# Optimization experiments

Measured on AMD Instinct MI355X. Metric: run time of the kernel, lower is better.

The kernel has to match this reference:

```python
import jax, jax.numpy as jnp
import numpy as np

N = 50000
E = 800000
F = 128
HID = 128
C = 40
GAMMA = 0.1
EPS = 0.1


def gcn(x, theta, src, dst, n):
    # GCNConv (bias=False) with added self-loops and symmetric normalization.
    xw = x @ theta  # [N, d]
    ones = jnp.ones(src.shape[0], dtype=x.dtype)
    deg = jax.ops.segment_sum(ones, dst, num_segments=n) + 1.0  # in-degree incl. self loop
    dinv = jax.lax.rsqrt(deg)
    norm = dinv[src] * dinv[dst]            # [E]
    msg = xw[src] * norm[:, None]           # [E, d]  (dominant memory traffic)
    agg = jax.ops.segment_sum(msg, dst, num_segments=n)
    return agg + xw * (dinv * dinv)[:, None]  # self-loop contribution


def antisym_conv(x, W, bias, theta, src, dst, n):
    # PyG AntiSymmetricConv, num_iters=1, act=tanh, eps=0.1, gamma=0.1
    M = W - W.T - GAMMA * jnp.eye(W.shape[0], dtype=x.dtype)
    h = gcn(x, theta, src, dst, n)
    h = x @ M.T + h + bias
    return x + EPS * jnp.tanh(h)


def setup_inputs() -> dict:
    key = jax.random.key(0)
    ks = jax.random.split(key, 12)
    s = 0.05
    return {
        "x": jax.random.normal(ks[0], (N, F), dtype=jnp.float32),
        "edge_index": jax.random.randint(ks[1], (2, E), 0, N, dtype=jnp.int64)
        if jax.config.jax_enable_x64 else jax.random.randint(ks[1], (2, E), 0, N, dtype=jnp.int32),
        # AntiSymmetricConv 1 (num_features channels)
        "W1": jax.random.normal(ks[2], (F, F), dtype=jnp.float32) * s,
        "b1": jnp.zeros((F,), dtype=jnp.float32),
        "T1": jax.random.normal(ks[3], (F, F), dtype=jnp.float32) * s,
        # AntiSymmetricConv 2 (nhid channels)
        "W2": jax.random.normal(ks[4], (HID, HID), dtype=jnp.float32) * s,
        "b2": jnp.zeros((HID,), dtype=jnp.float32),
        "T2": jax.random.normal(ks[5], (HID, HID), dtype=jnp.float32) * s,
        # Linear layers (torch convention: weight [out, in])
        "lw1": jax.random.normal(ks[6], (HID, F), dtype=jnp.float32) * s,
        "lb1": jnp.zeros((HID,), dtype=jnp.float32),
        "lw2": jax.random.normal(ks[7], (C, HID), dtype=jnp.float32) * s,
        "lb2": jnp.zeros((C,), dtype=jnp.float32),
    }


def reference(x, edge_index, W1, b1, T1, W2, b2, T2, lw1, lb1, lw2, lb2):
    src, dst = edge_index[0], edge_index[1]
    n = x.shape[0]
    # eval mode: dropout is identity
    h = antisym_conv(x, W1, b1, T1, src, dst, n)
    h = jax.nn.relu(h)
    h = h @ lw1.T + lb1
    h = jax.nn.relu(h)
    h = antisym_conv(h, W2, b2, T2, src, dst, n)
    h = jax.nn.relu(h)
    x1 = h
    logits = h @ lw2.T + lb2
    result = jax.nn.log_softmax(logits, axis=-1)
    return (result, x1)
```

## Files before the change

### kernel.cpp

```cpp
#include <hip/hip_runtime.h>
#include <hip/hip_bf16.h>
#include <math.h>

#define GAMMA_ 0.1f
#define EPS_ 0.1f
constexpr int BLK = 256;

typedef __attribute__((ext_vector_type(8))) short short8;
typedef __attribute__((ext_vector_type(4))) float f32x4;
typedef __attribute__((ext_vector_type(2))) float f32x2v;
typedef unsigned char u8;

__device__ inline float bflo(uint u) { union { uint i; float f; } v; v.i = u << 16; return v.f; }
__device__ inline float bfhi(uint u) { union { uint i; float f; } v; v.i = u & 0xffff0000u; return v.f; }
__device__ inline ushort f2bf(float f) {
  union { float f; uint i; } v; v.f = f;
  uint i = v.i;
  return (ushort)((i + 0x7fffu + ((i >> 16) & 1u)) >> 16);
}

#if __has_builtin(__builtin_amdgcn_cvt_pk_f32_fp8) && __has_builtin(__builtin_amdgcn_cvt_pk_fp8_f32)
#define HW_FP8 1
#endif

__device__ inline f32x2v fp8x2_dec_sw(uint raw) {
  f32x2v r;
#pragma unroll
  for (int i = 0; i < 2; ++i) {
    uint b = (raw >> (8 * i)) & 0xffu;
    uint em = b & 0x7fu;
    union { uint u; float f; } o;
    o.u = ((b & 0x80u) << 24) | (0x3C000000u + (em << 20));
    r[i] = (em >= 8u) ? o.f : 0.f;
  }
  return r;
}

__device__ inline f32x2v fp8x2_dec(uint raw) {
#ifdef HW_FP8
  return __builtin_amdgcn_cvt_pk_f32_fp8(raw, false);
#else
  return fp8x2_dec_sw(raw);
#endif
}

__device__ inline uint fp8enc1(float x) {
  union { float f; uint u; } v; v.f = x;
  uint s = (v.u >> 24) & 0x80u;
  uint a = v.u & 0x7fffffffu;
  if (a >= 0x43E00000u) return s | 0x7Eu;
  uint r = a + 0x7FFFFu + ((a >> 20) & 1u);
  if (r < 0x3D800000u) return s;
  return s | (((r - 0x3C000000u) >> 20) & 0x7fu);
}

template<bool HI>
__device__ inline uint fp8x2_enc(float f0, float f1, uint old) {
#ifdef HW_FP8
  return __builtin_amdgcn_cvt_pk_fp8_f32(f0, f1, old, HI);
#else
  uint p = fp8enc1(f0) | (fp8enc1(f1) << 8);
  return HI ? ((old & 0x0000ffffu) | (p << 16)) : ((old & 0xffff0000u) | p);
#endif
}

__global__ void k_count(const int* __restrict__ dst, int* cnt,
                        int* __restrict__ rank, int e) {
  int i = blockIdx.x * BLK + threadIdx.x;
  if (i < e) rank[i] = atomicAdd(&cnt[dst[i]], 1);
}

__global__ void k_scan1(const int* __restrict__ cnt, int* __restrict__ rowp,
                        int* __restrict__ bsum, int n) {
  __shared__ int s[BLK];
  int t = threadIdx.x;
  int i = blockIdx.x * BLK + t;
  int v = (i < n) ? cnt[i] : 0;
  s[t] = v; __syncthreads();
  for (int off = 1; off < BLK; off <<= 1) {
    int u = (t >= off) ? s[t - off] : 0;
    __syncthreads();
    s[t] += u;
    __syncthreads();
  }
  if (i < n) rowp[i] = s[t] - v;
  if (t == BLK - 1) bsum[blockIdx.x] = s[t];
}

__global__ void k_scan2(const int* __restrict__ bsum, int* __restrict__ boff, int nb) {
  __shared__ int s[BLK];
  int t = threadIdx.x;
  int v = (t < nb) ? bsum[t] : 0;
  s[t] = v; __syncthreads();
  for (int off = 1; off < BLK; off <<= 1) {
    int u = (t >= off) ? s[t - off] : 0;
    __syncthreads();
    s[t] += u;
    __syncthreads();
  }
  if (t < nb) boff[t] = s[t] - v;
}

__global__ void k_scan3(const int* __restrict__ boff, int* __restrict__ rowp,
                        const int* __restrict__ cnt, float* __restrict__ dinv,
                        int n, int e) {
  int i = blockIdx.x * BLK + threadIdx.x;
  if (i < n) {
    rowp[i] += boff[blockIdx.x];
    dinv[i] = rsqrtf((float)cnt[i] + 1.0f);
    if (i == 0) rowp[n] = e;
  }
}

__global__ void k_fill(const int* __restrict__ src, const int* __restrict__ dst,
                       const int* __restrict__ rowp, const int* __restrict__ rank,
                       int* __restrict__ csrc, int e) {
  int i = blockIdx.x * BLK + threadIdx.x;
  if (i < e) {
    int d = dst[i];
    csrc[rowp[d] + rank[i]] = src[i];
  }
}

__global__ void k_pack(const float* __restrict__ W1, const float* __restrict__ T1,
                       const float* __restrict__ W2, const float* __restrict__ T2,
                       const float* __restrict__ lw1, const float* __restrict__ lw2,
                       ushort* __restrict__ Bpk1, ushort* __restrict__ Bpk2,
                       ushort* __restrict__ Bpkl, ushort* __restrict__ Bpk2l) {
  int idx = blockIdx.x * BLK + threadIdx.x;
  if (idx < 65536) {
    int which = idx >> 15;
    int e = idx & 32767;
    int k = e >> 8, c = e & 255;
    const float* W = which ? W2 : W1;
    const float* T = which ? T2 : T1;
    float v;
    if (c < 128) {
      v = T[k * 128 + c];
    } else {
      int cc = c - 128;
      v = W[cc * 128 + k] - W[k * 128 + cc] - ((cc == k) ? GAMMA_ : 0.f);
    }
    int kt = k >> 5, q = (k >> 3) & 3, j = k & 7;
    ushort* B = which ? Bpk2 : Bpk1;
    B[(((kt * 4 + q) * 256 + c) << 3) + j] = f2bf(v);
  } else if (idx < 81920) {
    int e = idx - 65536;
    int k = e >> 7, c = e & 127;
    float v = lw1[c * 128 + k];
    int kt = k >> 5, q = (k >> 3) & 3, j = k & 7;
    Bpkl[(((kt * 4 + q) * 128 + c) << 3) + j] = f2bf(v);
  } else {
    int e = idx - 81920;
    if (e < 6144) {
      int k = e / 48, c = e - k * 48;
      float v = (c < 40) ? lw2[c * 128 + k] : 0.f;
      int kt = k >> 5, q = (k >> 3) & 3, j = k & 7;
      Bpk2l[(((kt * 4 + q) * 48 + c) << 3) + j] = f2bf(v);
    }
  }
}

__global__ __launch_bounds__(256) void k_mgemm(
    const float* __restrict__ Av, int nrows,
    const ushort* __restrict__ Bpk, const float* __restrict__ dinv,
    ushort* __restrict__ O1, u8* __restrict__ Oq) {
  __shared__ ushort S[64 * 256];
  const int t = threadIdx.x;
  const int w = t >> 6, l = t & 63;
  const int lr = l & 15, lq = l >> 4;
  const int r0 = blockIdx.x * 64;
#pragma unroll
  for (int it = 0; it < 4; ++it) {
    int chunk = it * 256 + t;
    int row = chunk >> 4, c16 = chunk & 15;
    int gr = min(r0 + row, nrows - 1);
    ushort* p = S + row * 128 + (c16 ^ (row & 7)) * 8;
    const float* A = Av + (size_t)gr * 128 + c16 * 8;
    float4 v0 = *(const float4*)(A);
    float4 v1 = *(const float4*)(A + 4);
    ushort4 o0 = {f2bf(v0.x), f2bf(v0.y), f2bf(v0.z), f2bf(v0.w)};
    ushort4 o1 = {f2bf(v1.x), f2bf(v1.y), f2bf(v1.z), f2bf(v1.w)};
    *(ushort4*)(p) = o0;
    *(ushort4*)(p + 4) = o1;
  }
  __syncthreads();
  f32x4 acc[4][4];
#pragma unroll
  for (int rt = 0; rt < 4; ++rt)
#pragma unroll
    for (int n = 0; n < 4; ++n) acc[rt][n] = f32x4{0.f, 0.f, 0.f, 0.f};
#pragma unroll
  for (int kt = 0; kt < 4; ++kt) {
    short8 af[4];
#pragma unroll
    for (int rt = 0; rt < 4; ++rt) {
      int row = rt * 16 + lr;
      af[rt] = *(const short8*)(S + row * 128 + ((kt * 4 + lq) ^ (row & 7)) * 8);
    }
    const ushort* bbase = Bpk + ((size_t)((kt * 4 + lq) * 256) + w * 64 + lr) * 8;
#pragma unroll
    for (int n = 0; n < 4; ++n) {
      short8 bf = *(const short8*)(bbase + n * 16 * 8);
#pragma unroll
      for (int rt = 0; rt < 4; ++rt)
        acc[rt][n] = __builtin_amdgcn_mfma_f32_16x16x32_bf16(af[rt], bf, acc[rt][n], 0, 0, 0);
    }
  }
  __syncthreads();
#pragma unroll
  for (int rt = 0; rt < 4; ++rt)
#pragma unroll
    for (int n = 0; n < 4; ++n)
#pragma unroll
      for (int r = 0; r < 4; ++r) {
        int row = rt * 16 + lq * 4 + r;
        int col = w * 64 + n * 16 + lr;
        int pcol = col ^ (((row >> 2) & 3) << 3);
        S[row * 256 + pcol] = f2bf(acc[rt][n][r]);
      }
  __syncthreads();
#pragma unroll
  for (int it = 0; it < 4; ++it) {
    int idx = it * 256 + t;
    int row = idx >> 4, c8 = idx & 15;
    if (r0 + row < nrows) {
      int pc = (16 + (c8 ^ ((row >> 2) & 3))) * 8;
      uint4 v = *(const uint4*)(S + row * 256 + pc);
      *(uint4*)(O1 + (size_t)(r0 + row) * 128 + c8 * 8) = v;
    }
  }
#pragma unroll
  for (int it = 0; it < 4; ++it) {
    int idx = it * 256 + t;
    int row = idx >> 4, c8 = idx & 15;
    if (r0 + row < nrows) {
      float di = dinv[r0 + row];
      int pc = (c8 ^ ((row >> 2) & 3)) * 8;
      const uint* p = (const uint*)(S + row * 256 + pc);
      uint u0 = p[0], u1 = p[1], u2 = p[2], u3 = p[3];
      uint lo = fp8x2_enc<false>(bflo(u0) * di, bfhi(u0) * di, 0u);
      lo = fp8x2_enc<true>(bflo(u1) * di, bfhi(u1) * di, lo);
      uint hi = fp8x2_enc<false>(bflo(u2) * di, bfhi(u2) * di, 0u);
      hi = fp8x2_enc<true>(bflo(u3) * di, bfhi(u3) * di, hi);
      uint2 ov = { lo, hi };
      *(uint2*)(Oq + (size_t)(r0 + row) * 128 + c8 * 8) = ov;
    }
  }
}

__device__ inline void gather_node(const u8* __restrict__ xq,
                                   const int* __restrict__ csrc,
                                   int e0, int e1, int l, int node,
                                   float& a0, float& a1) {
  uint su = *(const ushort*)(xq + (size_t)node * 128 + 2 * l);
  f32x2v sf = fp8x2_dec(su);
  a0 = sf[0]; a1 = sf[1];
  int e = e0;
  for (; e + 7 < e1; e += 8) {
    int s[8];
#pragma unroll
    for (int u = 0; u < 8; ++u) s[u] = csrc[e + u];
    uint g[8];
#pragma unroll
    for (int u = 0; u < 8; ++u)
      g[u] = *(const ushort*)(xq + (size_t)s[u] * 128 + 2 * l);
#pragma unroll
    for (int u = 0; u < 8; ++u) {
      f32x2v f = fp8x2_dec(g[u]);
      a0 += f[0]; a1 += f[1];
    }
  }
  if (e + 3 < e1) {
    int s[4];
#pragma unroll
    for (int u = 0; u < 4; ++u) s[u] = csrc[e + u];
    uint g[4];
#pragma unroll
    for (int u = 0; u < 4; ++u)
      g[u] = *(const ushort*)(xq + (size_t)s[u] * 128 + 2 * l);
#pragma unroll
    for (int u = 0; u < 4; ++u) {
      f32x2v f = fp8x2_dec(g[u]);
      a0 += f[0]; a1 += f[1];
    }
    e += 4;
  }
  for (; e < e1; ++e) {
    uint g0 = *(const ushort*)(xq + (size_t)csrc[e] * 128 + 2 * l);
    f32x2v f = fp8x2_dec(g0);
    a0 += f[0]; a1 += f[1];
  }
}

__global__ __launch_bounds__(512) void k_aggl(
    const u8* __restrict__ xq, const ushort* __restrict__ xmb,
    const float* __restrict__ xinf, const float* __restrict__ dinv,
    const int* __restrict__ rowp, const int* __restrict__ csrc,
    const float* __restrict__ bias, const ushort* __restrict__ Bpkl,
    const float* __restrict__ lb1, const ushort* __restrict__ Bpk2,
    ushort* __restrict__ h2b, ushort* __restrict__ xmb2, u8* __restrict__ xq2,
    int n) {
  __shared__ ushort S[32 * 256];
  ushort* Sa = S;
  ushort* Sb = S + 32 * 128;
  const int t = threadIdx.x;
  const int w = t >> 6, l = t & 63;
  const int lr = l & 15, lq = l >> 4;
  const int r0 = blockIdx.x * 32;
#pragma unroll
  for (int i = 0; i < 4; ++i) {
    int lrow = w * 4 + i;
    int node = r0 + lrow;
    float o0 = 0.f, o1 = 0.f;
    if (node < n) {
      float a0, a1;
      gather_node(xq, csrc, rowp[node], rowp[node + 1], l, node, a0, a1);
      float di = dinv[node];
      uint mu = *(const uint*)(xmb + (size_t)node * 128 + 2 * l);
      float h0 = a0 * di + bflo(mu) + bias[2 * l];
      float h1 = a1 * di + bfhi(mu) + bias[2 * l + 1];
      float2 xv = *(const float2*)(xinf + (size_t)node * 128 + 2 * l);
      o0 = fmaxf(xv.x + EPS_ * tanhf(h0), 0.f);
      o1 = fmaxf(xv.y + EPS_ * tanhf(h1), 0.f);
    }
    ushort2 o = { f2bf(o0), f2bf(o1) };
    *(ushort2*)(Sa + lrow * 128 + ((l >> 2) ^ (lrow & 7)) * 8 + (l & 3) * 2) = o;
  }
  __syncthreads();
  f32x4 acc[2];
  acc[0] = f32x4{0.f, 0.f, 0.f, 0.f};
  acc[1] = f32x4{0.f, 0.f, 0.f, 0.f};
#pragma unroll
  for (int kt = 0; kt < 4; ++kt) {
    short8 bf = *(const short8*)(Bpkl + ((size_t)((kt * 4 + lq) * 128) + w * 16 + lr) * 8);
#pragma unroll
    for (int rt = 0; rt < 2; ++rt) {
      int row = rt * 16 + lr;
      short8 af = *(const short8*)(Sa + row * 128 + ((kt * 4 + lq) ^ (row & 7)) * 8);
      acc[rt] = __builtin_amdgcn_mfma_f32_16x16x32_bf16(af, bf, acc[rt], 0, 0, 0);
    }
  }
  {
    int col = w * 16 + lr;
    float bv = lb1[col];
#pragma unroll
    for (int rt = 0; rt < 2; ++rt)
#pragma unroll
      for (int r = 0; r < 4; ++r) {
        int row = rt * 16 + lq * 4 + r;
        ushort hb = f2bf(fmaxf(acc[rt][r] + bv, 0.f));
        Sb[row * 128 + ((col >> 3) ^ (row & 7)) * 8 + (col & 7)] = hb;
      }
  }
  __syncthreads();
  {
    int row = t >> 4, c8 = t & 15;
    if (r0 + row < n) {
      uint4 v = *(const uint4*)(Sb + row * 128 + (c8 ^ (row & 7)) * 8);
      *(uint4*)(h2b + (size_t)(r0 + row) * 128 + c8 * 8) = v;
    }
  }
  f32x4 acc2[2][2];
#pragma unroll
  for (int rt = 0; rt < 2; ++rt)
#pragma unroll
    for (int ct = 0; ct < 2; ++ct) acc2[rt][ct] = f32x4{0.f, 0.f, 0.f, 0.f};
#pragma unroll
  for (int kt = 0; kt < 4; ++kt) {
    short8 af[2];
#pragma unroll
    for (int rt = 0; rt < 2; ++rt) {
      int row = rt * 16 + lr;
      af[rt] = *(const short8*)(Sb + row * 128 + ((kt * 4 + lq) ^ (row & 7)) * 8);
    }
#pragma unroll
    for (int ct = 0; ct < 2; ++ct) {
      const ushort* bb = Bpk2 + ((size_t)((kt * 4 + lq) * 256) + w * 32 + ct * 16 + lr) * 8;
      short8 bf = *(const short8*)bb;
#pragma unroll
      for (int rt = 0; rt < 2; ++rt)
        acc2[rt][ct] = __builtin_amdgcn_mfma_f32_16x16x32_bf16(af[rt], bf, acc2[rt][ct], 0, 0, 0);
    }
  }
  __syncthreads();
#pragma unroll
  for (int rt = 0; rt < 2; ++rt)
#pragma unroll
    for (int ct = 0; ct < 2; ++ct)
#pragma unroll
      for (int r = 0; r < 4; ++r) {
        int row = rt * 16 + lq * 4 + r;
        int col = w * 32 + ct * 16 + lr;
        int pcol = col ^ (((row >> 2) & 3) << 3);
        S[row * 256 + pcol] = f2bf(acc2[rt][ct][r]);
      }
  __syncthreads();
  {
    int row = t >> 4, c8 = t & 15;
    if (r0 + row < n) {
      int pc = (16 + (c8 ^ ((row >> 2) & 3))) * 8;
      uint4 v = *(const uint4*)(S + row * 256 + pc);
      *(uint4*)(xmb2 + (size_t)(r0 + row) * 128 + c8 * 8) = v;
      float di = dinv[r0 + row];
      int pq = (c8 ^ ((row >> 2) & 3)) * 8;
      const uint* p = (const uint*)(S + row * 256 + pq);
      uint u0 = p[0], u1 = p[1], u2 = p[2], u3 = p[3];
      uint lo = fp8x2_enc<false>(bflo(u0) * di, bfhi(u0) * di, 0u);
      lo = fp8x2_enc<true>(bflo(u1) * di, bfhi(u1) * di, lo);
      uint hi = fp8x2_enc<false>(bflo(u2) * di, bfhi(u2) * di, 0u);
      hi = fp8x2_enc<true>(bflo(u3) * di, bfhi(u3) * di, hi);
      uint2 ov = { lo, hi };
      *(uint2*)(xq2 + (size_t)(r0 + row) * 128 + c8 * 8) = ov;
    }
  }
}

__global__ __launch_bounds__(512) void k_aggf(
    const u8* __restrict__ xq, const ushort* __restrict__ xmb,
    const ushort* __restrict__ xinb, const float* __restrict__ dinv,
    const int* __restrict__ rowp, const int* __restrict__ csrc,
    const float* __restrict__ bias, const ushort* __restrict__ Bpk2l,
    const float* __restrict__ lb2,
    float* __restrict__ x1, float* __restrict__ outp, int n) {
  __shared__ ushort Sa[32 * 128];
  __shared__ float Ls[32 * 49];
  __shared__ float bl[48];
  const int t = threadIdx.x;
  if (t < 48) bl[t] = (t < 40) ? lb2[t] : 0.f;
  const int w = t >> 6, l = t & 63;
  const int lr = l & 15, lq = l >> 4;
  const int r0 = blockIdx.x * 32;
#pragma unroll
  for (int i = 0; i < 4; ++i) {
    int lrow = w * 4 + i;
    int node = r0 + lrow;
    float o0 = 0.f, o1 = 0.f;
    if (node < n) {
      float a0, a1;
      gather_node(xq, csrc, rowp[node], rowp[node + 1], l, node, a0, a1);
      float di = dinv[node];
      uint mu = *(const uint*)(xmb + (size_t)node * 128 + 2 * l);
      float h0 = a0 * di + bflo(mu) + bias[2 * l];
      float h1 = a1 * di + bfhi(mu) + bias[2 * l + 1];
      uint xu = *(const uint*)(xinb + (size_t)node * 128 + 2 * l);
      o0 = fmaxf(bflo(xu) + EPS_ * tanhf(h0), 0.f);
      o1 = fmaxf(bfhi(xu) + EPS_ * tanhf(h1), 0.f);
      float2 o = { o0, o1 };
      *(float2*)(x1 + (size_t)node * 128 + 2 * l) = o;
    }
    ushort2 ob = { f2bf(o0), f2bf(o1) };
    *(ushort2*)(Sa + lrow * 128 + ((l >> 2) ^ (lrow & 7)) * 8 + (l & 3) * 2) = ob;
  }
  __syncthreads();
  if (w < 6) {
    int rt = w / 3, ct = w % 3;
    f32x4 acc = f32x4{0.f, 0.f, 0.f, 0.f};
#pragma unroll
    for (int kt = 0; kt < 4; ++kt) {
      int row = rt * 16 + lr;
      short8 af = *(const short8*)(Sa + row * 128 + ((kt * 4 + lq) ^ (row & 7)) * 8);
      short8 bf = *(const short8*)(Bpk2l + ((size_t)((kt * 4 + lq) * 48) + ct * 16 + lr) * 8);
      acc = __builtin_amdgcn_mfma_f32_16x16x32_bf16(af, bf, acc, 0, 0, 0);
    }
#pragma unroll
    for (int r = 0; r < 4; ++r) {
      int row = rt * 16 + lq * 4 + r;
      int col = ct * 16 + lr;
      Ls[row * 49 + col] = acc[r] + bl[col];
    }
  }
  __syncthreads();
  if (t < 128) {
    int row = t >> 2, q = t & 3;
    if (r0 + row < n) {
      const float* Lr = Ls + row * 49 + q * 10;
      float m = -1e30f;
#pragma unroll
      for (int c = 0; c < 10; ++c) m = fmaxf(m, Lr[c]);
      m = fmaxf(m, __shfl_xor(m, 1));
      m = fmaxf(m, __shfl_xor(m, 2));
      float s = 0.f;
#pragma unroll
      for (int c = 0; c < 10; ++c) s += expf(Lr[c] - m);
      s += __shfl_xor(s, 1);
      s += __shfl_xor(s, 2);
      float lse = m + logf(s);
      float* Or = outp + (size_t)(r0 + row) * 40 + q * 10;
#pragma unroll
      for (int c = 0; c < 10; ++c) Or[c] = Lr[c] - lse;
    }
  }
}

extern "C" void kernel_launch(void* const* d_in, const int* in_sizes, int n_in,
                              void* d_out, int out_size, void* d_ws, size_t ws_size,
                              hipStream_t stream) {
  const float* x   = (const float*)d_in[0];
  const int*   ei  = (const int*)d_in[1];
  const float* W1  = (const float*)d_in[2];
  const float* b1  = (const float*)d_in[3];
  const float* T1  = (const float*)d_in[4];
  const float* W2  = (const float*)d_in[5];
  const float* b2  = (const float*)d_in[6];
  const float* T2  = (const float*)d_in[7];
  const float* lw1 = (const float*)d_in[8];
  const float* lb1 = (const float*)d_in[9];
  const float* lw2 = (const float*)d_in[10];
  const float* lb2 = (const float*)d_in[11];
  const int N = in_sizes[0] / 128;
  const int E = in_sizes[1] / 2;
  const int* src = ei;
  const int* dst = ei + E;

  float* ws = (float*)d_ws;
  size_t o = 0;
  float* dinv = ws;             o += N;
  int* cnt = (int*)(ws + o);    o += N;
  int* rowp = (int*)(ws + o);   o += (size_t)(N + 4);
  int* csrc = (int*)(ws + o);   o += E;
  int* rank = (int*)(ws + o);   o += E;
  int* bsum = (int*)(ws + o);   o += 256;
  int* boff = (int*)(ws + o);   o += 256;
  o = (o + 3) & ~(size_t)3;
  ushort* us = (ushort*)(ws + o);
  size_t uo = 0;
  ushort* Bpk1 = us + uo;       uo += 32768;
  ushort* Bpk2 = us + uo;       uo += 32768;
  ushort* Bpkl = us + uo;       uo += 16384;
  ushort* Bpk2l = us + uo;      uo += 6144;
  ushort* xmb  = us + uo;       uo += (size_t)N * 128;
  ushort* xmb2 = us + uo;       uo += (size_t)N * 128;
  ushort* h2b  = us + uo;       uo += (size_t)N * 128;
  u8* xq  = (u8*)(us + uo);     uo += (size_t)N * 64;
  u8* xq2 = (u8*)(us + uo);

  float* outp = (float*)d_out;
  float* x1 = outp + (size_t)N * 40;

  int nb_n = (N + BLK - 1) / BLK;
  int nb_e = (E + BLK - 1) / BLK;
  int nb_r = (N + 63) / 64;

  hipMemsetAsync(cnt, 0, (size_t)N * sizeof(int), stream);
  k_count<<<nb_e, BLK, 0, stream>>>(dst, cnt, rank, E);
  k_scan1<<<nb_n, BLK, 0, stream>>>(cnt, rowp, bsum, N);
  k_scan2<<<1, BLK, 0, stream>>>(bsum, boff, nb_n);
  k_scan3<<<nb_n, BLK, 0, stream>>>(boff, rowp, cnt, dinv, N, E);
  k_fill<<<nb_e, BLK, 0, stream>>>(src, dst, rowp, rank, csrc, E);
  k_pack<<<344, BLK, 0, stream>>>(W1, T1, W2, T2, lw1, lw2, Bpk1, Bpk2, Bpkl, Bpk2l);

  k_mgemm<<<nb_r, 256, 0, stream>>>(x, N, Bpk1, dinv, xmb, xq);
  k_aggl<<<(N + 31) / 32, 512, 0, stream>>>(
      xq, xmb, x, dinv, rowp, csrc, b1, Bpkl, lb1, Bpk2, h2b, xmb2, xq2, N);
  k_aggf<<<(N + 31) / 32, 512, 0, stream>>>(
      xq2, xmb2, h2b, dinv, rowp, csrc, b2, Bpk2l, lb2, x1, outp, N);
}
```

Baseline: 171.0 us.

## Split degree counters four ways and fuse CSR fill with first GEMM

Degree counting now uses four counter copies, picked by block index, to spread atomic contention. The scan turns these into per-copy offsets and also computes dinv. The memset is replaced by zeroing inside the pack kernel, and the CSR fill runs in the same launch as the first MFMA GEMM as extra blocks, cutting two launches. Gather addressing uses 32-bit shift/or instead of 64-bit multiply. The cost is four times the counter memory and an extra read in the fill path.

```diff
diff --git a/kernel.cpp b/kernel.cpp
--- a/kernel.cpp
+++ b/kernel.cpp
@@ -64,69 +64,12 @@
 #endif
 }
 
-__global__ void k_count(const int* __restrict__ dst, int* cnt,
-                        int* __restrict__ rank, int e) {
-  int i = blockIdx.x * BLK + threadIdx.x;
-  if (i < e) rank[i] = atomicAdd(&cnt[dst[i]], 1);
-}
-
-__global__ void k_scan1(const int* __restrict__ cnt, int* __restrict__ rowp,
-                        int* __restrict__ bsum, int n) {
-  __shared__ int s[BLK];
-  int t = threadIdx.x;
-  int i = blockIdx.x * BLK + t;
-  int v = (i < n) ? cnt[i] : 0;
-  s[t] = v; __syncthreads();
-  for (int off = 1; off < BLK; off <<= 1) {
-    int u = (t >= off) ? s[t - off] : 0;
-    __syncthreads();
-    s[t] += u;
-    __syncthreads();
-  }
-  if (i < n) rowp[i] = s[t] - v;
-  if (t == BLK - 1) bsum[blockIdx.x] = s[t];
-}
-
-__global__ void k_scan2(const int* __restrict__ bsum, int* __restrict__ boff, int nb) {
-  __shared__ int s[BLK];
-  int t = threadIdx.x;
-  int v = (t < nb) ? bsum[t] : 0;
-  s[t] = v; __syncthreads();
-  for (int off = 1; off < BLK; off <<= 1) {
-    int u = (t >= off) ? s[t - off] : 0;
-    __syncthreads();
-    s[t] += u;
-    __syncthreads();
-  }
-  if (t < nb) boff[t] = s[t] - v;
-}
-
-__global__ void k_scan3(const int* __restrict__ boff, int* __restrict__ rowp,
-                        const int* __restrict__ cnt, float* __restrict__ dinv,
-                        int n, int e) {
-  int i = blockIdx.x * BLK + threadIdx.x;
-  if (i < n) {
-    rowp[i] += boff[blockIdx.x];
-    dinv[i] = rsqrtf((float)cnt[i] + 1.0f);
-    if (i == 0) rowp[n] = e;
-  }
-}
-
-__global__ void k_fill(const int* __restrict__ src, const int* __restrict__ dst,
-                       const int* __restrict__ rowp, const int* __restrict__ rank,
-                       int* __restrict__ csrc, int e) {
-  int i = blockIdx.x * BLK + threadIdx.x;
-  if (i < e) {
-    int d = dst[i];
-    csrc[rowp[d] + rank[i]] = src[i];
-  }
-}
-
 __global__ void k_pack(const float* __restrict__ W1, const float* __restrict__ T1,
                        const float* __restrict__ W2, const float* __restrict__ T2,
                        const float* __restrict__ lw1, const float* __restrict__ lw2,
                        ushort* __restrict__ Bpk1, ushort* __restrict__ Bpk2,
-                       ushort* __restrict__ Bpkl, ushort* __restrict__ Bpk2l) {
+                       ushort* __restrict__ Bpkl, ushort* __restrict__ Bpk2l,
+                       int* __restrict__ cnt4, int n4) {
   int idx = blockIdx.x * BLK + threadIdx.x;
   if (idx < 65536) {
     int which = idx >> 15;
@@ -150,26 +93,95 @@
     float v = lw1[c * 128 + k];
     int kt = k >> 5, q = (k >> 3) & 3, j = k & 7;
     Bpkl[(((kt * 4 + q) * 128 + c) << 3) + j] = f2bf(v);
+  } else if (idx < 88064) {
+    int e = idx - 81920;
+    int k = e / 48, c = e - k * 48;
+    float v = (c < 40) ? lw2[c * 128 + k] : 0.f;
+    int kt = k >> 5, q = (k >> 3) & 3, j = k & 7;
+    Bpk2l[(((kt * 4 + q) * 48 + c) << 3) + j] = f2bf(v);
   } else {
-    int e = idx - 81920;
-    if (e < 6144) {
-      int k = e / 48, c = e - k * 48;
-      float v = (c < 40) ? lw2[c * 128 + k] : 0.f;
-      int kt = k >> 5, q = (k >> 3) & 3, j = k & 7;
-      Bpk2l[(((kt * 4 + q) * 48 + c) << 3) + j] = f2bf(v);
-    }
-  }
-}
-
-__global__ __launch_bounds__(256) void k_mgemm(
-    const float* __restrict__ Av, int nrows,
-    const ushort* __restrict__ Bpk, const float* __restrict__ dinv,
+    int i = idx - 88064;
+    if (i < n4) cnt4[i] = 0;
+  }
+}
+
+__global__ void k_count4(const int* __restrict__ dst, int* __restrict__ cnt4,
+                         int* __restrict__ rank, int e, int n) {
+  int i = blockIdx.x * BLK + threadIdx.x;
+  int c = blockIdx.x & 3;
+  if (i < e) rank[i] = atomicAdd(&cnt4[c * n + dst[i]], 1);
+}
+
+__global__ void k_scan1(int* __restrict__ cnt4, int* __restrict__ rowp,
+                        int* __restrict__ bsum, float* __restrict__ dinv, int n) {
+  __shared__ int s[BLK];
+  int t = threadIdx.x;
+  int i = blockIdx.x * BLK + t;
+  int tot = 0;
+  if (i < n) {
+    int c0 = cnt4[i], c1 = cnt4[n + i], c2 = cnt4[2 * n + i], c3 = cnt4[3 * n + i];
+    tot = c0 + c1 + c2 + c3;
+    cnt4[i] = 0;
+    cnt4[n + i] = c0;
+    cnt4[2 * n + i] = c0 + c1;
+    cnt4[3 * n + i] = c0 + c1 + c2;
+    dinv[i] = rsqrtf((float)tot + 1.0f);
+  }
+  s[t] = tot; __syncthreads();
+  for (int off = 1; off < BLK; off <<= 1) {
+    int u = (t >= off) ? s[t - off] : 0;
+    __syncthreads();
+    s[t] += u;
+    __syncthreads();
+  }
+  if (i < n) rowp[i] = s[t] - tot;
+  if (t == BLK - 1) bsum[blockIdx.x] = s[t];
+}
+
+__global__ void k_scan2(const int* __restrict__ bsum, int* __restrict__ boff, int nb) {
+  __shared__ int s[BLK];
+  int t = threadIdx.x;
+  int v = (t < nb) ? bsum[t] : 0;
+  s[t] = v; __syncthreads();
+  for (int off = 1; off < BLK; off <<= 1) {
+    int u = (t >= off) ? s[t - off] : 0;
+    __syncthreads();
+    s[t] += u;
+    __syncthreads();
+  }
+  if (t < nb) boff[t] = s[t] - v;
+}
+
+__global__ void k_scan3(const int* __restrict__ boff, int* __restrict__ rowp,
+                        int n, int e) {
+  int i = blockIdx.x * BLK + threadIdx.x;
+  if (i < n) {
+    rowp[i] += boff[blockIdx.x];
+    if (i == 0) rowp[n] = e;
+  }
+}
+
+__global__ __launch_bounds__(256) void k_fm(
+    const int* __restrict__ src, const int* __restrict__ dst,
+    const int* __restrict__ rowp, const int* __restrict__ rank,
+    const int* __restrict__ cnt4, int* __restrict__ csrc, int e, int nbf, int n,
+    const float* __restrict__ Av, int nrows, const ushort* __restrict__ Bpk,
+    const float* __restrict__ dinv,
     ushort* __restrict__ O1, u8* __restrict__ Oq) {
   __shared__ ushort S[64 * 256];
+  if ((int)blockIdx.x < nbf) {
+    int i = blockIdx.x * BLK + threadIdx.x;
+    if (i < e) {
+      int d = dst[i];
+      int c = blockIdx.x & 3;
+      csrc[rowp[d] + cnt4[c * n + d] + rank[i]] = src[i];
+    }
+    return;
+  }
   const int t = threadIdx.x;
   const int w = t >> 6, l = t & 63;
   const int lr = l & 15, lq = l >> 4;
-  const int r0 = blockIdx.x * 64;
+  const int r0 = ((int)blockIdx.x - nbf) * 64;
 #pragma unroll
   for (int it = 0; it < 4; ++it) {
     int chunk = it * 256 + t;
@@ -189,7 +201,7 @@
 #pragma unroll
   for (int rt = 0; rt < 4; ++rt)
 #pragma unroll
-    for (int n = 0; n < 4; ++n) acc[rt][n] = f32x4{0.f, 0.f, 0.f, 0.f};
+    for (int n2 = 0; n2 < 4; ++n2) acc[rt][n2] = f32x4{0.f, 0.f, 0.f, 0.f};
 #pragma unroll
   for (int kt = 0; kt < 4; ++kt) {
     short8 af[4];
@@ -200,24 +212,24 @@
     }
     const ushort* bbase = Bpk + ((size_t)((kt * 4 + lq) * 256) + w * 64 + lr) * 8;
 #pragma unroll
-    for (int n = 0; n < 4; ++n) {
-      short8 bf = *(const short8*)(bbase + n * 16 * 8);
+    for (int n2 = 0; n2 < 4; ++n2) {
+      short8 bf = *(const short8*)(bbase + n2 * 16 * 8);
 #pragma unroll
       for (int rt = 0; rt < 4; ++rt)
-        acc[rt][n] = __builtin_amdgcn_mfma_f32_16x16x32_bf16(af[rt], bf, acc[rt][n], 0, 0, 0);
+        acc[rt][n2] = __builtin_amdgcn_mfma_f32_16x16x32_bf16(af[rt], bf, acc[rt][n2], 0, 0, 0);
     }
   }
   __syncthreads();
 #pragma unroll
   for (int rt = 0; rt < 4; ++rt)
 #pragma unroll
-    for (int n = 0; n < 4; ++n)
+    for (int n2 = 0; n2 < 4; ++n2)
 #pragma unroll
       for (int r = 0; r < 4; ++r) {
         int row = rt * 16 + lq * 4 + r;
-        int col = w * 64 + n * 16 + lr;
+        int col = w * 64 + n2 * 16 + lr;
         int pcol = col ^ (((row >> 2) & 3) << 3);
-        S[row * 256 + pcol] = f2bf(acc[rt][n][r]);
+        S[row * 256 + pcol] = f2bf(acc[rt][n2][r]);
       }
   __syncthreads();
 #pragma unroll
@@ -253,7 +265,8 @@
                                    const int* __restrict__ csrc,
                                    int e0, int e1, int l, int node,
                                    float& a0, float& a1) {
-  uint su = *(const ushort*)(xq + (size_t)node * 128 + 2 * l);
+  const uint fo = 2u * (uint)l;
+  uint su = *(const ushort*)(xq + ((((uint)node) << 7) | fo));
   f32x2v sf = fp8x2_dec(su);
   a0 = sf[0]; a1 = sf[1];
   int e = e0;
@@ -264,7 +277,7 @@
     uint g[8];
 #pragma unroll
     for (int u = 0; u < 8; ++u)
-      g[u] = *(const ushort*)(xq + (size_t)s[u] * 128 + 2 * l);
+      g[u] = *(const ushort*)(xq + ((((uint)s[u]) << 7) | fo));
 #pragma unroll
     for (int u = 0; u < 8; ++u) {
       f32x2v f = fp8x2_dec(g[u]);
@@ -278,7 +291,7 @@
     uint g[4];
 #pragma unroll
     for (int u = 0; u < 4; ++u)
-      g[u] = *(const ushort*)(xq + (size_t)s[u] * 128 + 2 * l);
+      g[u] = *(const ushort*)(xq + ((((uint)s[u]) << 7) | fo));
 #pragma unroll
     for (int u = 0; u < 4; ++u) {
       f32x2v f = fp8x2_dec(g[u]);
@@ -287,7 +300,7 @@
     e += 4;
   }
   for (; e < e1; ++e) {
-    uint g0 = *(const ushort*)(xq + (size_t)csrc[e] * 128 + 2 * l);
+    uint g0 = *(const ushort*)(xq + ((((uint)csrc[e]) << 7) | fo));
     f32x2v f = fp8x2_dec(g0);
     a0 += f[0]; a1 += f[1];
   }
@@ -516,7 +529,7 @@
   float* ws = (float*)d_ws;
   size_t o = 0;
   float* dinv = ws;             o += N;
-  int* cnt = (int*)(ws + o);    o += N;
+  int* cnt4 = (int*)(ws + o);   o += (size_t)4 * N;
   int* rowp = (int*)(ws + o);   o += (size_t)(N + 4);
   int* csrc = (int*)(ws + o);   o += E;
   int* rank = (int*)(ws + o);   o += E;
@@ -541,16 +554,16 @@
   int nb_n = (N + BLK - 1) / BLK;
   int nb_e = (E + BLK - 1) / BLK;
   int nb_r = (N + 63) / 64;
-
-  hipMemsetAsync(cnt, 0, (size_t)N * sizeof(int), stream);
-  k_count<<<nb_e, BLK, 0, stream>>>(dst, cnt, rank, E);
-  k_scan1<<<nb_n, BLK, 0, stream>>>(cnt, rowp, bsum, N);
+  int nb_pack = (88064 + 4 * N + BLK - 1) / BLK;
+
+  k_pack<<<nb_pack, BLK, 0, stream>>>(W1, T1, W2, T2, lw1, lw2,
+                                      Bpk1, Bpk2, Bpkl, Bpk2l, cnt4, 4 * N);
+  k_count4<<<nb_e, BLK, 0, stream>>>(dst, cnt4, rank, E, N);
+  k_scan1<<<nb_n, BLK, 0, stream>>>(cnt4, rowp, bsum, dinv, N);
   k_scan2<<<1, BLK, 0, stream>>>(bsum, boff, nb_n);
-  k_scan3<<<nb_n, BLK, 0, stream>>>(boff, rowp, cnt, dinv, N, E);
-  k_fill<<<nb_e, BLK, 0, stream>>>(src, dst, rowp, rank, csrc, E);
-  k_pack<<<344, BLK, 0, stream>>>(W1, T1, W2, T2, lw1, lw2, Bpk1, Bpk2, Bpkl, Bpk2l);
-
-  k_mgemm<<<nb_r, 256, 0, stream>>>(x, N, Bpk1, dinv, xmb, xq);
+  k_scan3<<<nb_n, BLK, 0, stream>>>(boff, rowp, N, E);
+  k_fm<<<nb_e + nb_r, BLK, 0, stream>>>(src, dst, rowp, rank, cnt4, csrc, E, nb_e, N,
+                                        x, N, Bpk1, dinv, xmb, xq);
   k_aggl<<<(N + 31) / 32, 512, 0, stream>>>(
       xq, xmb, x, dinv, rowp, csrc, b1, Bpkl, lb1, Bpk2, h2b, xmb2, xq2, N);
   k_aggf<<<(N + 31) / 32, 512, 0, stream>>>(
```

Measured after the change: 164.9 us. 3.6% less time.
